# Performance work log

Hardware: AMD Instinct MI355X
Metric: run time of the kernel (lower is better)

Reference implementation:

```python
import jax, jax.numpy as jnp
import numpy as np
from jax import lax

# model dims (must match init_kwargs)
NB, E, G0, G1 = 1, 64, 32, 256          # num_blocks, embed_dim, grid rows, grid cols
DM, DIN, DS, DC, DTR = 2048, 4096, 16, 4, 128  # d_model, d_inner, d_state, d_conv, dt_rank
PS, ST, KD = (2, 16), (2, 16), (31, 31)
B, C, T = 8, 64, 4096


def setup_inputs() -> dict:
    key = jax.random.key(0)
    ks = jax.random.split(key, 4)
    rng = np.random.default_rng(0)

    def w(*s, fan=None):
        fan = fan if fan is not None else s[-1]
        return jnp.asarray((rng.standard_normal(s) / np.sqrt(fan)).astype(np.float32))

    # mamba_ssm-style dt bias init: softplus(bias) ~ Uniform-log in [1e-3, 0.1]
    dt = np.exp(rng.uniform(size=(NB, 2, DIN)) * (np.log(0.1) - np.log(1e-3)) + np.log(1e-3))
    dt = np.clip(dt, 1e-4, None)
    bdt = jnp.asarray((dt + np.log(-np.expm1(-dt))).astype(np.float32))
    A_log = jnp.asarray(np.broadcast_to(np.log(np.arange(1, DS + 1, dtype=np.float32)), (NB, 2, DIN, DS)).copy())

    return {
        'x': jax.random.normal(ks[0], (B, C, T), dtype=jnp.float32),
        'mask': jax.random.uniform(ks[1], (B, C, T)) < 0.5,
        'proj_w': w(E, 1, PS[0], PS[1], fan=PS[0] * PS[1]),
        'proj_b': jnp.zeros((E,), jnp.float32),
        'pos_embed': 0.02 * jax.random.normal(ks[2], (1, G1, DM), dtype=jnp.float32),
        'in_proj_w': w(NB, 2, 2 * DIN, DM, fan=DM),
        'conv_w': w(NB, 2, DIN, DC, fan=DC),
        'conv_b': jnp.zeros((NB, 2, DIN), jnp.float32),
        'x_proj_w': w(NB, 2, DTR + 2 * DS, DIN, fan=DIN),
        'dt_proj_w': w(NB, 2, DIN, DTR, fan=DTR),
        'dt_proj_b': bdt,
        'A_log': A_log,
        'Dp': jnp.ones((NB, 2, DIN), jnp.float32),
        'out_proj_w': w(NB, 2, DM, DIN, fan=DIN),
        'ln_g': jnp.ones((NB, DM), jnp.float32),
        'ln_b': jnp.zeros((NB, DM), jnp.float32),
        'dec_conv_w': w(1, 1, KD[0], KD[1], fan=KD[0] * KD[1]),
        'convT_w': w(E, 1, PS[0], PS[1], fan=E),
        'convT_b': jnp.zeros((1,), jnp.float32),
    }


def _layernorm(x, g, b, eps=1e-5):
    m = jnp.mean(x, -1, keepdims=True)
    v = jnp.var(x, -1, keepdims=True)
    return (x - m) * lax.rsqrt(v + eps) * g + b


def _mamba(h, Win, Wc, bc, Wx, Wdt, bdt, Alog, Dp, Wout):
    # h: [B, L, DM]; faithful port of mamba_ssm Mamba (selective scan reference path)
    xz = jnp.einsum('bld,ed->ble', h, Win)               # [B, L, 2*DIN]
    xc, z = jnp.split(xz, 2, axis=-1)
    xc = xc.swapaxes(1, 2)                               # [B, DIN, L]
    xc = lax.conv_general_dilated(xc, Wc[:, None, :], (1,), ((DC - 1, 0),),
                                  dimension_numbers=('NCH', 'OIH', 'NCH'),
                                  feature_group_count=DIN) + bc[None, :, None]
    u = jax.nn.silu(xc).swapaxes(1, 2)                   # [B, L, DIN]
    x_dbl = jnp.einsum('bld,ed->ble', u, Wx)             # [B, L, DTR+2*DS]
    dt = jax.nn.softplus(jnp.einsum('blr,dr->bld', x_dbl[..., :DTR], Wdt) + bdt)
    Bm = x_dbl[..., DTR:DTR + DS]                        # [B, L, DS]
    Cm = x_dbl[..., DTR + DS:]                           # [B, L, DS]
    A = -jnp.exp(Alog)                                   # [DIN, DS]

    def step(hst, inp):
        dt_t, B_t, C_t, u_t = inp                        # [B,DIN],[B,DS],[B,DS],[B,DIN]
        dA = jnp.exp(dt_t[..., None] * A)                # [B, DIN, DS]
        hst = hst * dA + (dt_t * u_t)[..., None] * B_t[:, None, :]
        return hst, jnp.einsum('bds,bs->bd', hst, C_t)

    h0 = jnp.zeros((h.shape[0], DIN, DS), h.dtype)
    xs = (dt.swapaxes(0, 1), Bm.swapaxes(0, 1), Cm.swapaxes(0, 1), u.swapaxes(0, 1))
    _, ys = lax.scan(step, h0, xs)
    y = ys.swapaxes(0, 1) + u * Dp                       # [B, L, DIN]
    y = y * jax.nn.silu(z)
    return jnp.einsum('bld,ed->ble', y, Wout)            # [B, L, DM]


def _forward(x, mask, proj_w, proj_b, pos_embed, in_proj_w, conv_w, conv_b,
             x_proj_w, dt_proj_w, dt_proj_b, A_log, Dp, out_proj_w,
             ln_g, ln_b, dec_conv_w, convT_w, convT_b):
    xm = jnp.where(mask, 0.0, x)                         # x_masked[mask] = 0
    p = lax.conv_general_dilated(xm[:, None], proj_w, ST, 'VALID',
                                 dimension_numbers=('NCHW', 'OIHW', 'NCHW'))
    p = p + proj_b[None, :, None, None]                  # [B, E, G0, G1]
    h = p.reshape(p.shape[0], E * G0, G1).transpose(0, 2, 1) + pos_embed  # [B, G1, DM]
    for i in range(NB):
        a_f = (in_proj_w[i, 0], conv_w[i, 0], conv_b[i, 0], x_proj_w[i, 0], dt_proj_w[i, 0],
               dt_proj_b[i, 0], A_log[i, 0], Dp[i, 0], out_proj_w[i, 0])
        a_r = (in_proj_w[i, 1], conv_w[i, 1], conv_b[i, 1], x_proj_w[i, 1], dt_proj_w[i, 1],
               dt_proj_b[i, 1], A_log[i, 1], Dp[i, 1], out_proj_w[i, 1])
        o = _mamba(h, *a_f) + jnp.flip(_mamba(jnp.flip(h, 1), *a_r), 1)  # bidirectional add
        h = _layernorm(h + o, ln_g[i], ln_b[i])
    # Decoder
    d = lax.conv_general_dilated(h[:, None], dec_conv_w, (1, 1),
                                 (((KD[0] - 1) // 2,) * 2, ((KD[1] - 1) // 2,) * 2),
                                 dimension_numbers=('NCHW', 'OIHW', 'NCHW'))
    d = d[:, 0].transpose(0, 2, 1).reshape(-1, E, G0, G1)
    # ConvTranspose2d(E->1, k=PS, stride=ST) as lhs-dilated conv with flipped kernel
    wct = jnp.flip(convT_w, (2, 3)).swapaxes(0, 1)       # [1, E, kh, kw]
    rec = lax.conv_general_dilated(d, wct, (1, 1),
                                   ((PS[0] - 1, PS[0] - 1), (PS[1] - 1, PS[1] - 1)),
                                   lhs_dilation=ST,
                                   dimension_numbers=('NCHW', 'OIHW', 'NCHW'))
    rec = rec + convT_b[None, :, None, None]
    return rec[:, 0], x                                  # (x_reconstructed, x_original)


def reference(x, mask, proj_w, proj_b, pos_embed, in_proj_w, conv_w, conv_b,
              x_proj_w, dt_proj_w, dt_proj_b, A_log, Dp, out_proj_w,
              ln_g, ln_b, dec_conv_w, convT_w, convT_b):
    return _forward(x, mask, proj_w, proj_b, pos_embed, in_proj_w, conv_w, conv_b,
                    x_proj_w, dt_proj_w, dt_proj_b, A_log, Dp, out_proj_w,
                    ln_g, ln_b, dec_conv_w, convT_w, convT_b)
```

## Files before the change

### kernel.cpp

```cpp
#include <hip/hip_runtime.h>
#include <hip/hip_bf16.h>
#include <math.h>

typedef unsigned short u16;
typedef __attribute__((ext_vector_type(8))) short bf16x8;
typedef __attribute__((ext_vector_type(4))) float f32x4;

__device__ __forceinline__ float b2f(u16 v) {
  unsigned u = ((unsigned)v) << 16;
  return __builtin_bit_cast(float, u);
}
__device__ __forceinline__ u16 f2b(float f) {
  unsigned u = __builtin_bit_cast(unsigned, f);
  unsigned r = u + 0x7fffu + ((u >> 16) & 1u);
  return (u16)(r >> 16);
}
__device__ __forceinline__ void gload_lds16(const u16* g, u16* l) {
  __builtin_amdgcn_global_load_lds(
      (const __attribute__((address_space(1))) void*)g,
      (__attribute__((address_space(3))) void*)l, 16, 0, 0);
}

__global__ __launch_bounds__(256) void cvt_bf16_k(const float* __restrict__ s,
                                                  u16* __restrict__ d, int n4) {
  int i = blockIdx.x * 256 + threadIdx.x;
  if (i < n4) {
    float4 v = ((const float4*)s)[i];
    ushort4 o;
    o.x = f2b(v.x); o.y = f2b(v.y); o.z = f2b(v.z); o.w = f2b(v.w);
    ((ushort4*)d)[i] = o;
  }
}

__global__ __launch_bounds__(256) void patchify_k(
    const float* __restrict__ x, const int* __restrict__ mask,
    const float* __restrict__ pw, const float* __restrict__ pb,
    const float* __restrict__ pos, float* __restrict__ h, u16* __restrict__ hb)
{
  int g1 = blockIdx.x, b = blockIdx.y, tid = threadIdx.x;
  __shared__ float sX[64 * 17];
  __shared__ float sW[2048];
  for (int i = tid; i < 64 * 16; i += 256) {
    int r = i >> 4, c = i & 15;
    int gi = (b * 64 + r) * 4096 + g1 * 16 + c;
    sX[r * 17 + c] = mask[gi] ? 0.f : x[gi];
  }
  for (int i = tid; i < 2048; i += 256) sW[i] = pw[i];
  __syncthreads();
  for (int m = tid; m < 2048; m += 256) {
    int e = m >> 5, g0 = m & 31;
    float acc = pb[e];
    const float* w = &sW[e * 32];
#pragma unroll
    for (int kh = 0; kh < 2; ++kh)
#pragma unroll
      for (int kw = 0; kw < 16; ++kw)
        acc += sX[(2 * g0 + kh) * 17 + kw] * w[kh * 16 + kw];
    float v = acc + pos[g1 * 2048 + m];
    long o = ((long)b * 256 + g1) * 2048 + m;
    h[o] = v;
    hb[o] = f2b(v);
  }
}

__global__ __launch_bounds__(512, 2) void gemm256_k(
    const u16* __restrict__ A0,
    const u16* __restrict__ B0, long bStride,
    u16* __restrict__ C0, long cStride,
    const float* __restrict__ cw,
    const float* __restrict__ cb,
    u16* __restrict__ ub)
{
  constexpr int K = 2048, N = 8192, LDA = 2048;
  __shared__ __align__(16) u16 lds[67584];
  u16* As = lds;
  u16* Bs = lds + 32768;
  const int dir = blockIdx.z;
  const u16* A = A0;
  const u16* B = B0 + (long)dir * bStride;
  u16* C = C0 + (long)dir * cStride;
  const int flip = dir;

  const int tid = threadIdx.x;
  const int wave = tid >> 6, lane = tid & 63;
  const int wr = wave >> 2, wc = wave & 3;
  const int bm = blockIdx.y * 256, bn = blockIdx.x * 256;
  const int lr = lane & 15, lq = lane >> 4;

  f32x4 acc[8][4];
#pragma unroll
  for (int i = 0; i < 8; ++i)
#pragma unroll
    for (int j = 0; j < 4; ++j) acc[i][j] = (f32x4){0.f, 0.f, 0.f, 0.f};

  auto stage = [&](int buf, int kt) {
    int k0 = kt << 6;
#pragma unroll
    for (int hf = 0; hf < 2; ++hf)
#pragma unroll
      for (int j = 0; j < 2; ++j) {
        int g = j * 512 + tid;
        int rl = hf * 128 + (g >> 3);
        int gr = (g & 7) ^ ((g >> 3) & 7);
        int ar = flip ? (bm + 255 - rl) : (bm + rl);
        gload_lds16(A + (long)ar * LDA + k0 + gr * 8,
                    &As[buf * 16384 + hf * 8192 + g * 8]);
        gload_lds16(B + (long)(bn + rl) * K + k0 + gr * 8,
                    &Bs[buf * 16384 + hf * 8192 + g * 8]);
      }
  };

  const int nk = K >> 6;
  stage(0, 0);
  for (int kt = 0; kt < nk; ++kt) {
    __builtin_amdgcn_s_barrier();
    __builtin_amdgcn_sched_barrier(0);
    if (kt + 1 < nk) {
      stage((kt + 1) & 1, kt + 1);
      asm volatile("s_waitcnt vmcnt(16)" ::: "memory");
    } else {
      asm volatile("s_waitcnt vmcnt(0)" ::: "memory");
    }
    __builtin_amdgcn_sched_barrier(0);
    __builtin_amdgcn_s_barrier();
    __builtin_amdgcn_sched_barrier(0);
    const int buf = kt & 1;
#pragma unroll
    for (int h = 0; h < 2; ++h) {
      bf16x8 av[8], bv[4];
#pragma unroll
      for (int i = 0; i < 8; ++i) {
        int row = wr * 128 + i * 16 + lr;
        av[i] = *(const bf16x8*)
            &As[buf * 16384 + ((row * 64 + h * 32 + lq * 8) ^ ((row & 7) << 3))];
      }
#pragma unroll
      for (int j = 0; j < 4; ++j) {
        int row = wc * 64 + j * 16 + lr;
        bv[j] = *(const bf16x8*)
            &Bs[buf * 16384 + ((row * 64 + h * 32 + lq * 8) ^ ((row & 7) << 3))];
      }
      __builtin_amdgcn_s_setprio(1);
#pragma unroll
      for (int i = 0; i < 8; ++i)
#pragma unroll
        for (int j = 0; j < 4; ++j)
          acc[i][j] = __builtin_amdgcn_mfma_f32_16x16x32_bf16(
              av[i], bv[j], acc[i][j], 0, 0, 0);
      __builtin_amdgcn_s_setprio(0);
    }
  }

  if (bn < 4096) {
    __syncthreads();
    u16* tile = lds;
#pragma unroll
    for (int i = 0; i < 8; ++i) {
      int r0 = wr * 128 + i * 16 + lq * 4;
#pragma unroll
      for (int j = 0; j < 4; ++j) {
        int col = wc * 64 + j * 16 + lr;
        f32x4 v = acc[i][j];
#pragma unroll
        for (int r = 0; r < 4; ++r)
          tile[(r0 + r) * 264 + col] = f2b(v[r]);
      }
    }
    __syncthreads();
    const int rgrp = tid >> 5, c8 = tid & 31;
    const int d0 = bn + c8 * 8;
    float wv0[8], wv1[8], wv2[8], wv3[8], cbv[8];
#pragma unroll
    for (int e = 0; e < 8; ++e) {
      const float4 wq = *(const float4*)(cw + ((long)dir * 4096 + d0 + e) * 4);
      wv0[e] = wq.x; wv1[e] = wq.y; wv2[e] = wq.z; wv3[e] = wq.w;
      cbv[e] = cb[dir * 4096 + d0 + e];
    }
    const int l0 = rgrp * 16;
    float w0[8], w1[8], w2[8];
#pragma unroll
    for (int e = 0; e < 8; ++e) { w0[e] = 0.f; w1[e] = 0.f; w2[e] = 0.f; }
    if (rgrp > 0) {
      bf16x8 t0 = *(const bf16x8*)&tile[(l0 - 3) * 264 + c8 * 8];
      bf16x8 t1 = *(const bf16x8*)&tile[(l0 - 2) * 264 + c8 * 8];
      bf16x8 t2 = *(const bf16x8*)&tile[(l0 - 1) * 264 + c8 * 8];
#pragma unroll
      for (int e = 0; e < 8; ++e) {
        w0[e] = b2f((u16)t0[e]); w1[e] = b2f((u16)t1[e]); w2[e] = b2f((u16)t2[e]);
      }
    }
    long ubase = ((long)(dir * 8 + blockIdx.y) * 256 + l0) * 4096 + d0;
#pragma unroll
    for (int l = 0; l < 16; ++l) {
      bf16x8 t = *(const bf16x8*)&tile[(l0 + l) * 264 + c8 * 8];
      float cur[8];
#pragma unroll
      for (int e = 0; e < 8; ++e) cur[e] = b2f((u16)t[e]);
      bf16x8 ov;
#pragma unroll
      for (int e = 0; e < 8; ++e) {
        float a = cbv[e] + wv0[e] * w0[e] + wv1[e] * w1[e] + wv2[e] * w2[e] +
                  wv3[e] * cur[e];
        ov[e] = (short)f2b(a / (1.f + __expf(-a)));
      }
      *(bf16x8*)(ub + ubase + (long)l * 4096) = ov;
#pragma unroll
      for (int e = 0; e < 8; ++e) { w0[e] = w1[e]; w1[e] = w2[e]; w2[e] = cur[e]; }
    }
  } else {
#pragma unroll
    for (int i = 0; i < 8; ++i) {
      int r0 = bm + wr * 128 + i * 16 + lq * 4;
#pragma unroll
      for (int j = 0; j < 4; ++j) {
        int col = bn + wc * 64 + j * 16 + lr;
        f32x4 v = acc[i][j];
#pragma unroll
        for (int r = 0; r < 4; ++r)
          C[(long)(r0 + r) * N + col] = f2b(v[r]);
      }
    }
  }
}

template <int EPI, int F32OUT, int BFOUT>
__global__ __launch_bounds__(256) void mfma_gemm_k(
    const u16* __restrict__ A0, long aStride,
    const u16* __restrict__ B0, long bStride,
    float* __restrict__ C0, long cStride,
    u16* __restrict__ Cb0, long cbStride,
    const float* __restrict__ bias0, int biasStride,
    int N, int K, int lda, int flipDir1)
{
  __shared__ __align__(16) u16 As[2][4096];
  __shared__ __align__(16) u16 Bs[2][4096];
  const int dir = blockIdx.z;
  const u16* A = A0 + (long)dir * aStride;
  const u16* B = B0 + (long)dir * bStride;
  float* C = F32OUT ? (C0 + (long)dir * cStride) : nullptr;
  u16* Cb = BFOUT ? (Cb0 + (long)dir * cbStride) : nullptr;
  const float* bias = (EPI == 1) ? (bias0 + (long)dir * biasStride) : nullptr;
  const int flip = flipDir1 && (dir == 1);

  const int tid = threadIdx.x;
  const int wave = tid >> 6, lane = tid & 63;
  const int wr = wave >> 1, wc = wave & 1;
  const int bm = blockIdx.y * 128, bn = blockIdx.x * 128;
  const int lr = lane & 15, lq = lane >> 4;

  f32x4 acc[4][4];
#pragma unroll
  for (int i = 0; i < 4; ++i)
#pragma unroll
    for (int j = 0; j < 4; ++j) acc[i][j] = (f32x4){0.f, 0.f, 0.f, 0.f};

  const int nk = K >> 5;

  auto stage = [&](int buf, int k0) {
#pragma unroll
    for (int iss = 0; iss < 2; ++iss) {
      int ob = wave * 2048 + iss * 1024 + lane * 16;
      int row = ob >> 6, kb = (ob >> 4) & 3;
      int rg = bm + row;
      rg = flip ? ((rg & ~255) | (255 - (rg & 255))) : rg;
      gload_lds16(A + (long)rg * lda + k0 + kb * 8,
                  &As[buf][wave * 1024 + iss * 512]);
      int rb = bn + row; rb = (rb < N) ? rb : (N - 1);
      gload_lds16(B + (long)rb * K + k0 + kb * 8,
                  &Bs[buf][wave * 1024 + iss * 512]);
    }
  };

  stage(0, 0);
  for (int kt = 0; kt < nk; ++kt) {
    __syncthreads();
    if (kt + 1 < nk) stage((kt + 1) & 1, (kt + 1) << 5);
    const int buf = kt & 1;
    bf16x8 av[4], bv[4];
#pragma unroll
    for (int i = 0; i < 4; ++i)
      av[i] = *(const bf16x8*)&As[buf][(wr * 64 + i * 16 + lr) * 32 + lq * 8];
#pragma unroll
    for (int j = 0; j < 4; ++j)
      bv[j] = *(const bf16x8*)&Bs[buf][(wc * 64 + j * 16 + lr) * 32 + lq * 8];
#pragma unroll
    for (int i = 0; i < 4; ++i)
#pragma unroll
      for (int j = 0; j < 4; ++j)
        acc[i][j] = __builtin_amdgcn_mfma_f32_16x16x32_bf16(av[i], bv[j],
                                                            acc[i][j], 0, 0, 0);
  }

#pragma unroll
  for (int i = 0; i < 4; ++i) {
    int r0 = bm + wr * 64 + i * 16 + lq * 4;
#pragma unroll
    for (int j = 0; j < 4; ++j) {
      int col = bn + wc * 64 + j * 16 + lr;
      if (col < N) {
        f32x4 v = acc[i][j];
#pragma unroll
        for (int r = 0; r < 4; ++r) {
          float xv = v[r];
          if (EPI == 1) {
            xv += bias[col];
            xv = (xv > 20.f) ? xv : log1pf(expf(xv));
          }
          if (F32OUT) C[(long)(r0 + r) * N + col] = xv;
          if (BFOUT) Cb[(long)(r0 + r) * N + col] = f2b(xv);
        }
      }
    }
  }
}

__global__ __launch_bounds__(256) void xdbl_part_k(
    const u16* __restrict__ ubf, const u16* __restrict__ Wxbf,
    float* __restrict__ part)
{
  __shared__ __align__(16) u16 As[2][4096];
  __shared__ __align__(16) u16 Bs[2][4096];
  const int dir = blockIdx.z >> 2, split = blockIdx.z & 3;
  const u16* A = ubf + (long)dir * 2048 * 4096;
  const u16* B = Wxbf + (long)dir * 160 * 4096;
  float* C = part + (long)blockIdx.z * 327680;
  const int tid = threadIdx.x;
  const int wave = tid >> 6, lane = tid & 63;
  const int wr = wave >> 1, wc = wave & 1;
  const int bm = blockIdx.y * 128, bn = blockIdx.x * 128;
  const int lr = lane & 15, lq = lane >> 4;

  f32x4 acc[4][4];
#pragma unroll
  for (int i = 0; i < 4; ++i)
#pragma unroll
    for (int j = 0; j < 4; ++j) acc[i][j] = (f32x4){0.f, 0.f, 0.f, 0.f};

  auto stage = [&](int buf, int k0) {
#pragma unroll
    for (int iss = 0; iss < 2; ++iss) {
      int ob = wave * 2048 + iss * 1024 + lane * 16;
      int row = ob >> 6, kb = (ob >> 4) & 3;
      gload_lds16(A + (long)(bm + row) * 4096 + k0 + kb * 8,
                  &As[buf][wave * 1024 + iss * 512]);
      int rb = bn + row; rb = (rb < 160) ? rb : 159;
      gload_lds16(B + (long)rb * 4096 + k0 + kb * 8,
                  &Bs[buf][wave * 1024 + iss * 512]);
    }
  };

  const int kbase = split << 10;
  stage(0, kbase);
  for (int kt = 0; kt < 32; ++kt) {
    __syncthreads();
    if (kt + 1 < 32) stage((kt + 1) & 1, kbase + ((kt + 1) << 5));
    const int buf = kt & 1;
    bf16x8 av[4], bv[4];
#pragma unroll
    for (int i = 0; i < 4; ++i)
      av[i] = *(const bf16x8*)&As[buf][(wr * 64 + i * 16 + lr) * 32 + lq * 8];
#pragma unroll
    for (int j = 0; j < 4; ++j)
      bv[j] = *(const bf16x8*)&Bs[buf][(wc * 64 + j * 16 + lr) * 32 + lq * 8];
#pragma unroll
    for (int i = 0; i < 4; ++i)
#pragma unroll
      for (int j = 0; j < 4; ++j)
        acc[i][j] = __builtin_amdgcn_mfma_f32_16x16x32_bf16(av[i], bv[j],
                                                            acc[i][j], 0, 0, 0);
  }

#pragma unroll
  for (int i = 0; i < 4; ++i) {
    int r0 = bm + wr * 64 + i * 16 + lq * 4;
#pragma unroll
    for (int j = 0; j < 4; ++j) {
      int col = bn + wc * 64 + j * 16 + lr;
      if (col < 160) {
        f32x4 v = acc[i][j];
#pragma unroll
        for (int r = 0; r < 4; ++r)
          C[(long)(r0 + r) * 160 + col] = v[r];
      }
    }
  }
}

__global__ __launch_bounds__(256) void xdbl_reduce_k(
    const float* __restrict__ part, float* __restrict__ xdbl,
    u16* __restrict__ xdbl_bf)
{
  int i = blockIdx.x * 256 + threadIdx.x;
  if (i >= 655360) return;
  int dir = i / 327680, rem = i - dir * 327680;
  long pb = (long)dir * 4 * 327680 + rem;
  float s = part[pb] + part[pb + 327680] + part[pb + 2 * 327680] +
            part[pb + 3 * 327680];
  xdbl[i] = s;
  xdbl_bf[i] = f2b(s);
}

__global__ __launch_bounds__(256) void scan_a_k(
    const u16* __restrict__ dtbuf, const u16* __restrict__ ubuf,
    const float* __restrict__ xdbl, const float* __restrict__ A_log,
    const float* __restrict__ Dpv, u16* __restrict__ ypre,
    float* __restrict__ stend, float* __restrict__ dtsum)
{
  int blk = blockIdx.x;
  int dtile = blk & 15, c = (blk >> 4) & 7, b = (blk >> 7) & 7, dir = blk >> 10;
  int tid = threadIdx.x;
  int d = dtile * 256 + tid;
  int db = dir * 8 + b;

  __shared__ float sB[32][16], sC[32][16];
  long r160 = (long)db * 256 * 160;
  for (int i = tid; i < 1024; i += 256) {
    int l = i >> 5, s = i & 31;
    float v = xdbl[r160 + (long)(c * 32 + l) * 160 + 128 + s];
    if (s < 16) sB[l][s] = v; else sC[l][s - 16] = v;
  }
  __syncthreads();

  float A[16], st[16];
  const float4* ap = (const float4*)(A_log + ((long)dir * 4096 + d) * 16);
#pragma unroll
  for (int q = 0; q < 4; ++q) {
    float4 t = ap[q];
    A[q * 4 + 0] = -__expf(t.x); A[q * 4 + 1] = -__expf(t.y);
    A[q * 4 + 2] = -__expf(t.z); A[q * 4 + 3] = -__expf(t.w);
  }
#pragma unroll
  for (int s = 0; s < 16; ++s) st[s] = 0.f;
  float Dpd = Dpv[dir * 4096 + d];

  long base = (long)db * 256 * 4096 + (long)c * 32 * 4096 + d;
  float dts = 0.f;
  for (int i = 0; i < 32; ++i) {
    float dtv = b2f(dtbuf[base + (long)i * 4096]);
    float uv  = b2f(ubuf[base + (long)i * 4096]);
    dts += dtv;
    float du = dtv * uv;
    float y = 0.f;
#pragma unroll
    for (int s = 0; s < 16; ++s) {
      st[s] = st[s] * __expf(dtv * A[s]) + du * sB[i][s];
      y += st[s] * sC[i][s];
    }
    ypre[base + (long)i * 4096] = f2b(y + uv * Dpd);
  }
  long eb = ((long)(db * 8 + c) * 4096 + d) * 16;
  float4* ep = (float4*)(stend + eb);
#pragma unroll
  for (int q = 0; q < 4; ++q)
    ep[q] = make_float4(st[q * 4], st[q * 4 + 1], st[q * 4 + 2], st[q * 4 + 3]);
  dtsum[(long)(db * 8 + c) * 4096 + d] = dts;
}

__global__ __launch_bounds__(512) void scan_b_k(
    const u16* __restrict__ dtbuf, const u16* __restrict__ xzbf,
    const float* __restrict__ xdbl, const float* __restrict__ A_log,
    const float* __restrict__ stend, const float* __restrict__ dtsum,
    u16* __restrict__ ybuf)
{
  int blk = blockIdx.x;
  int dtile = blk & 63, b = (blk >> 6) & 7, dir = blk >> 9;
  int tid = threadIdx.x;
  int c = tid >> 6, dd = tid & 63;
  int d0 = dtile * 64, d = d0 + dd;
  int db = dir * 8 + b;

  __shared__ float sEnd[8][64][17];
  __shared__ float sT[8][64];
  __shared__ float sC[256][16];

  long eBase = (long)db * 8 * 65536;
  for (int i = tid; i < 8192; i += 512) {
    int cc = i >> 10, rem = i & 1023, dd2 = rem >> 4, s = rem & 15;
    sEnd[cc][dd2][s] = stend[eBase + (long)cc * 65536 + (long)(d0 + dd2) * 16 + s];
  }
  {
    int cc = tid >> 6, dd2 = tid & 63;
    sT[cc][dd2] = dtsum[(long)(db * 8 + cc) * 4096 + d0 + dd2];
  }
  long r160 = (long)db * 256 * 160;
  for (int i = tid; i < 4096; i += 512) {
    int l = i >> 4, s = i & 15;
    sC[l][s] = xdbl[r160 + (long)l * 160 + 144 + s];
  }
  __syncthreads();

  float A[16];
  const float4* ap = (const float4*)(A_log + ((long)dir * 4096 + d) * 16);
#pragma unroll
  for (int q = 0; q < 4; ++q) {
    float4 t = ap[q];
    A[q * 4 + 0] = -__expf(t.x); A[q * 4 + 1] = -__expf(t.y);
    A[q * 4 + 2] = -__expf(t.z); A[q * 4 + 3] = -__expf(t.w);
  }
  float g[16];
#pragma unroll
  for (int s = 0; s < 16; ++s) g[s] = 0.f;
  for (int j = 0; j < c; ++j) {
    float Tj = sT[j][dd];
#pragma unroll
    for (int s = 0; s < 16; ++s)
      g[s] = g[s] * __expf(A[s] * Tj) + sEnd[j][dd][s];
  }

  long base  = (long)db * 256 * 4096 + (long)c * 32 * 4096 + d;
  long zbase = (long)db * 256 * 8192 + (long)c * 32 * 8192 + 4096 + d;
  float cum = 0.f;
  if (c == 0) {
    for (int i = 0; i < 32; ++i) {
      float yp = b2f(ybuf[base + (long)i * 4096]);
      float zv = b2f(xzbf[zbase + (long)i * 8192]);
      float y = yp * (zv / (1.f + __expf(-zv)));
      ybuf[base + (long)i * 4096] = f2b(y);
    }
  } else {
    for (int i = 0; i < 32; ++i) {
      float dtv = b2f(dtbuf[base + (long)i * 4096]);
      cum += dtv;
      float yp = b2f(ybuf[base + (long)i * 4096]);
      float corr = 0.f;
      const int l = c * 32 + i;
#pragma unroll
      for (int s = 0; s < 16; ++s)
        corr += sC[l][s] * __expf(A[s] * cum) * g[s];
      float zv = b2f(xzbf[zbase + (long)i * 8192]);
      float y = (yp + corr) * (zv / (1.f + __expf(-zv)));
      ybuf[base + (long)i * 4096] = f2b(y);
    }
  }
}

__global__ __launch_bounds__(256) void add_ln_k(
    const float* __restrict__ h, const float* __restrict__ o0,
    const float* __restrict__ o1, const float* __restrict__ g,
    const float* __restrict__ bta, float* __restrict__ h2)
{
  int row = blockIdx.x;
  int b = row >> 8, l = row & 255;
  long base = (long)row * 2048;
  long base1 = ((long)b * 256 + (255 - l)) * 2048;
  int t8 = threadIdx.x * 8;
  float v[8];
  float4 x0 = *(const float4*)(h + base + t8);
  float4 x1 = *(const float4*)(h + base + t8 + 4);
  float4 a0 = *(const float4*)(o0 + base + t8);
  float4 a1 = *(const float4*)(o0 + base + t8 + 4);
  float4 c0 = *(const float4*)(o1 + base1 + t8);
  float4 c1 = *(const float4*)(o1 + base1 + t8 + 4);
  v[0] = x0.x + a0.x + c0.x; v[1] = x0.y + a0.y + c0.y;
  v[2] = x0.z + a0.z + c0.z; v[3] = x0.w + a0.w + c0.w;
  v[4] = x1.x + a1.x + c1.x; v[5] = x1.y + a1.y + c1.y;
  v[6] = x1.z + a1.z + c1.z; v[7] = x1.w + a1.w + c1.w;
  float s = 0.f, ss = 0.f;
#pragma unroll
  for (int j = 0; j < 8; ++j) { s += v[j]; ss += v[j] * v[j]; }
#pragma unroll
  for (int off = 32; off >= 1; off >>= 1) {
    s += __shfl_xor(s, off, 64);
    ss += __shfl_xor(ss, off, 64);
  }
  __shared__ float red[8];
  int wid = threadIdx.x >> 6, lane = threadIdx.x & 63;
  if (lane == 0) { red[wid] = s; red[wid + 4] = ss; }
  __syncthreads();
  if (threadIdx.x == 0) {
    red[0] = red[0] + red[1] + red[2] + red[3];
    red[4] = red[4] + red[5] + red[6] + red[7];
  }
  __syncthreads();
  float mean = red[0] * (1.f / 2048.f);
  float var = red[4] * (1.f / 2048.f) - mean * mean;
  float inv = rsqrtf(var + 1e-5f);
  float o[8];
#pragma unroll
  for (int j = 0; j < 8; ++j)
    o[j] = (v[j] - mean) * inv * g[t8 + j] + bta[t8 + j];
  *(float4*)(h2 + base + t8) = make_float4(o[0], o[1], o[2], o[3]);
  *(float4*)(h2 + base + t8 + 4) = make_float4(o[4], o[5], o[6], o[7]);
}

__global__ __launch_bounds__(256) void dec_conv31_k(
    const float* __restrict__ h2, const float* __restrict__ kw,
    float* __restrict__ dc)
{
  __shared__ u16 sIn[62 * 168];
  __shared__ float sKw[961];
  int b = blockIdx.z;
  int l0 = blockIdx.y * 32;
  int m0 = blockIdx.x * 128;
  int tid = threadIdx.x;
  const float* src = h2 + (long)b * 256 * 2048;
  for (int i = tid; i < 961; i += 256) sKw[i] = kw[i];
  for (int i = tid; i < 62 * 168; i += 256) {
    int r = i / 168, c = i - r * 168;
    int gl = l0 + r - 15, gm = m0 + c - 15;
    float v = 0.f;
    if (c < 158 && gl >= 0 && gl < 256 && gm >= 0 && gm < 2048)
      v = src[(long)gl * 2048 + gm];
    sIn[i] = f2b(v);
  }
  __syncthreads();
  int tx = tid & 15, ty = tid >> 4;
  float acc[2][8];
#pragma unroll
  for (int r = 0; r < 2; ++r)
#pragma unroll
    for (int c = 0; c < 8; ++c) acc[r][c] = 0.f;

#pragma unroll 1
  for (int k = 0; k < 32; ++k) {
    const u16* rowp = &sIn[(ty * 2 + k) * 168 + tx * 8];
    float w[40];
#pragma unroll
    for (int q = 0; q < 5; ++q) {
      bf16x8 t = *(const bf16x8*)(rowp + q * 8);
#pragma unroll
      for (int e = 0; e < 8; ++e) w[q * 8 + e] = b2f((u16)t[e]);
    }
#pragma unroll
    for (int r = 0; r < 2; ++r) {
      unsigned ki = (unsigned)(k - r);
      if (ki > 30u) continue;
      const float* kwr = &sKw[ki * 31];
#pragma unroll
      for (int kj = 0; kj < 31; ++kj) {
        float kv = kwr[kj];
#pragma unroll
        for (int c = 0; c < 8; ++c) acc[r][c] += w[kj + c] * kv;
      }
    }
  }
#pragma unroll
  for (int r = 0; r < 2; ++r) {
    long obase = ((long)b * 256 + l0 + ty * 2 + r) * 2048 + m0 + tx * 8;
    *(float4*)(dc + obase) = make_float4(acc[r][0], acc[r][1], acc[r][2], acc[r][3]);
    *(float4*)(dc + obase + 4) = make_float4(acc[r][4], acc[r][5], acc[r][6], acc[r][7]);
  }
}

__global__ __launch_bounds__(256) void convT_k(
    const float* __restrict__ dc, const float* __restrict__ w,
    const float* __restrict__ wb, float* __restrict__ out)
{
  int j = blockIdx.x, b = blockIdx.y;
  __shared__ float sD[2048];
  __shared__ float sW[2048];
  int tid = threadIdx.x;
  const float* drow = dc + ((long)b * 256 + j) * 2048;
  for (int i = tid; i < 2048; i += 256) { sD[i] = drow[i]; sW[i] = w[i]; }
  __syncthreads();
  float cb = wb[0];
  int owlo = tid & 15, ohbase = tid >> 4;
#pragma unroll
  for (int q = 0; q < 4; ++q) {
    int oh = ohbase + q * 16;
    int i = oh >> 1, a = oh & 1;
    float acc = cb;
#pragma unroll 8
    for (int e = 0; e < 64; ++e)
      acc += sD[e * 32 + i] * sW[e * 32 + a * 16 + owlo];
    out[((long)b * 64 + oh) * 4096 + j * 16 + owlo] = acc;
  }
}

extern "C" void kernel_launch(void* const* d_in, const int* in_sizes, int n_in,
                              void* d_out, int out_size, void* d_ws, size_t ws_size,
                              hipStream_t stream)
{
  const float* x      = (const float*)d_in[0];
  const int*   mask   = (const int*)d_in[1];
  const float* proj_w = (const float*)d_in[2];
  const float* proj_b = (const float*)d_in[3];
  const float* pos    = (const float*)d_in[4];
  const float* Wip    = (const float*)d_in[5];
  const float* convw  = (const float*)d_in[6];
  const float* convb  = (const float*)d_in[7];
  const float* Wx     = (const float*)d_in[8];
  const float* Wdt    = (const float*)d_in[9];
  const float* bdt    = (const float*)d_in[10];
  const float* Alog   = (const float*)d_in[11];
  const float* Dpv    = (const float*)d_in[12];
  const float* Wout   = (const float*)d_in[13];
  const float* lng    = (const float*)d_in[14];
  const float* lnb    = (const float*)d_in[15];
  const float* dkw    = (const float*)d_in[16];
  const float* ctw    = (const float*)d_in[17];
  const float* ctb    = (const float*)d_in[18];
  float* out = (float*)d_out;

  char* p = (char*)d_ws;
  u16*   xz_bf   = (u16*)p;
  float* ob      = (float*)p;
  p += 67108864;
  u16*   u_bf    = (u16*)p;
  float* dc      = (float*)p;
  p += 33554432;
  u16*   dt_bf   = (u16*)p; p += 67108864;
  float* xdbl    = (float*)p; p += 2621440;
  u16*   xdbl_bf = (u16*)p;  p += 1310720;
  float* h       = (float*)p; p += 16777216;
  u16*   h_bf    = (u16*)p;  p += 8388608;
  float* h2      = (float*)p; p += 16777216;
  u16*   y_bf    = (u16*)p;  p += 33554432;
  u16*   Wpool   = (u16*)p;  p += 67108864;
  u16*   Wx_bf   = (u16*)p;  p += 2621440;
  u16*   Wdt_bf  = (u16*)p;  p += 2097152;

  float* part   = (float*)(Wpool + 16777216);
  float* st_end = (float*)(Wpool + 16777216);
  float* dtsum  = h2;

  cvt_bf16_k<<<32768, 256, 0, stream>>>(Wip, Wpool, 8388608);
  cvt_bf16_k<<<1280, 256, 0, stream>>>(Wx, Wx_bf, 327680);
  cvt_bf16_k<<<1024, 256, 0, stream>>>(Wdt, Wdt_bf, 262144);

  patchify_k<<<dim3(256, 8), 256, 0, stream>>>(x, mask, proj_w, proj_b, pos, h, h_bf);

  gemm256_k<<<dim3(32, 8, 2), 512, 0, stream>>>(
      h_bf, Wpool, (long)8192 * 2048, xz_bf, (long)2048 * 8192,
      convw, convb, u_bf);

  xdbl_part_k<<<dim3(2, 16, 8), 256, 0, stream>>>(u_bf, Wx_bf, part);
  xdbl_reduce_k<<<2560, 256, 0, stream>>>(part, xdbl, xdbl_bf);

  mfma_gemm_k<1, 0, 1><<<dim3(32, 16, 2), 256, 0, stream>>>(
      xdbl_bf, (long)2048 * 160, Wdt_bf, (long)4096 * 128, nullptr, 0L,
      dt_bf, (long)2048 * 4096, bdt, 4096, 4096, 128, 160, 0);

  scan_a_k<<<2048, 256, 0, stream>>>(dt_bf, u_bf, xdbl, Alog, Dpv, y_bf, st_end, dtsum);
  scan_b_k<<<1024, 512, 0, stream>>>(dt_bf, xz_bf, xdbl, Alog, st_end, dtsum, y_bf);

  cvt_bf16_k<<<16384, 256, 0, stream>>>(Wout, Wpool, 4194304);

  mfma_gemm_k<0, 1, 0><<<dim3(16, 16, 2), 256, 0, stream>>>(
      y_bf, (long)2048 * 4096, Wpool, (long)2048 * 4096, ob, (long)2048 * 2048,
      nullptr, 0L, nullptr, 0, 2048, 4096, 4096, 0);

  add_ln_k<<<2048, 256, 0, stream>>>(h, ob, ob + (long)2048 * 2048, lng, lnb, h2);

  dec_conv31_k<<<dim3(16, 8, 8), 256, 0, stream>>>(h2, dkw, dc);

  convT_k<<<dim3(256, 8), 256, 0, stream>>>(dc, ctw, ctb, out);

  hipMemcpyAsync(out + 2097152, x, (size_t)2097152 * 4,
                 hipMemcpyDeviceToDevice, stream);
}
```

Before: 690.4 us.

## Fuse dt projection GEMM with chunked scan pass and store cumulative dt

The dt_proj GEMM (with bias and softplus) is merged into the first scan kernel. Each 128x128 MFMA tile's softplus output stays in LDS and feeds the per-chunk selective scan directly, so the full bf16 dt tensor is never written and read back. The kernel instead writes a bf16 cumulative-dt array that the second scan pass reads in place of recomputing running sums, which also removes the separate dtsum buffer. Costs: each thread now scans two chunks in sequence with fewer blocks in flight, and the cumulative sums are rounded to bf16, which may lose precision in the correction exponent.

```diff
diff --git a/kernel.cpp b/kernel.cpp
--- a/kernel.cpp
+++ b/kernel.cpp
@@ -400,67 +400,144 @@
   xdbl_bf[i] = f2b(s);
 }
 
-__global__ __launch_bounds__(256) void scan_a_k(
-    const u16* __restrict__ dtbuf, const u16* __restrict__ ubuf,
+__global__ __launch_bounds__(256) void dtscan_k(
+    const u16* __restrict__ xdblbf, const u16* __restrict__ Wdtbf,
+    const float* __restrict__ bdt, const u16* __restrict__ ubuf,
     const float* __restrict__ xdbl, const float* __restrict__ A_log,
     const float* __restrict__ Dpv, u16* __restrict__ ypre,
-    float* __restrict__ stend, float* __restrict__ dtsum)
-{
-  int blk = blockIdx.x;
-  int dtile = blk & 15, c = (blk >> 4) & 7, b = (blk >> 7) & 7, dir = blk >> 10;
-  int tid = threadIdx.x;
-  int d = dtile * 256 + tid;
-  int db = dir * 8 + b;
-
-  __shared__ float sB[32][16], sC[32][16];
+    u16* __restrict__ cumdt, float* __restrict__ stend)
+{
+  __shared__ __align__(16) u16 lds[25088];
+  u16* As = lds;
+  u16* Bs = lds + 8192;
+  const int dir = blockIdx.z;
+  const u16* A = xdblbf + (long)dir * 2048 * 160;
+  const u16* B = Wdtbf + (long)dir * 4096 * 128;
+  const float* bias = bdt + dir * 4096;
+  const int tid = threadIdx.x;
+  const int wave = tid >> 6, lane = tid & 63;
+  const int wr = wave >> 1, wc = wave & 1;
+  const int bm = blockIdx.y * 128, bn = blockIdx.x * 128;
+  const int lr = lane & 15, lq = lane >> 4;
+
+  f32x4 acc[4][4];
+#pragma unroll
+  for (int i = 0; i < 4; ++i)
+#pragma unroll
+    for (int j = 0; j < 4; ++j) acc[i][j] = (f32x4){0.f, 0.f, 0.f, 0.f};
+
+  auto stage = [&](int buf, int k0) {
+#pragma unroll
+    for (int iss = 0; iss < 2; ++iss) {
+      int ob = wave * 2048 + iss * 1024 + lane * 16;
+      int row = ob >> 6, kb = (ob >> 4) & 3;
+      gload_lds16(A + (long)(bm + row) * 160 + k0 + kb * 8,
+                  &As[buf * 4096 + wave * 1024 + iss * 512]);
+      gload_lds16(B + (long)(bn + row) * 128 + k0 + kb * 8,
+                  &Bs[buf * 4096 + wave * 1024 + iss * 512]);
+    }
+  };
+
+  stage(0, 0);
+  for (int kt = 0; kt < 4; ++kt) {
+    __syncthreads();
+    if (kt + 1 < 4) stage((kt + 1) & 1, (kt + 1) << 5);
+    const int buf = kt & 1;
+    bf16x8 av[4], bv[4];
+#pragma unroll
+    for (int i = 0; i < 4; ++i)
+      av[i] = *(const bf16x8*)&As[buf * 4096 + (wr * 64 + i * 16 + lr) * 32 + lq * 8];
+#pragma unroll
+    for (int j = 0; j < 4; ++j)
+      bv[j] = *(const bf16x8*)&Bs[buf * 4096 + (wc * 64 + j * 16 + lr) * 32 + lq * 8];
+#pragma unroll
+    for (int i = 0; i < 4; ++i)
+#pragma unroll
+      for (int j = 0; j < 4; ++j)
+        acc[i][j] = __builtin_amdgcn_mfma_f32_16x16x32_bf16(av[i], bv[j],
+                                                            acc[i][j], 0, 0, 0);
+  }
+
+  __syncthreads();
+  u16* tile = lds;
+  float* sB = (float*)(lds + 16896);
+  float* sC = sB + 2048;
+#pragma unroll
+  for (int i = 0; i < 4; ++i) {
+    int r0 = wr * 64 + i * 16 + lq * 4;
+#pragma unroll
+    for (int j = 0; j < 4; ++j) {
+      int col = wc * 64 + j * 16 + lr;
+      f32x4 v = acc[i][j];
+#pragma unroll
+      for (int r = 0; r < 4; ++r) {
+        float xv = v[r] + bias[bn + col];
+        xv = (xv > 20.f) ? xv : log1pf(expf(xv));
+        tile[(r0 + r) * 132 + col] = f2b(xv);
+      }
+    }
+  }
+
+  const int db = dir * 8 + (bm >> 8);
+  const int l0 = bm & 255;
+  const int c0 = l0 >> 5;
   long r160 = (long)db * 256 * 160;
-  for (int i = tid; i < 1024; i += 256) {
-    int l = i >> 5, s = i & 31;
-    float v = xdbl[r160 + (long)(c * 32 + l) * 160 + 128 + s];
-    if (s < 16) sB[l][s] = v; else sC[l][s - 16] = v;
+  for (int i2 = tid; i2 < 2048; i2 += 256) {
+    int row = i2 >> 4, s = i2 & 15;
+    float2 bc = *(const float2*)&xdbl[r160 + (long)(l0 + row) * 160 + 128 + s * 2];
+    (void)bc;
+    sB[row * 16 + s] = xdbl[r160 + (long)(l0 + row) * 160 + 128 + s];
+    sC[row * 16 + s] = xdbl[r160 + (long)(l0 + row) * 160 + 144 + s];
   }
   __syncthreads();
 
-  float A[16], st[16];
-  const float4* ap = (const float4*)(A_log + ((long)dir * 4096 + d) * 16);
+  const int d_loc = tid & 127, half = tid >> 7;
+  const int d_glob = bn + d_loc;
+  float Aa[16];
+  const float4* ap = (const float4*)(A_log + ((long)dir * 4096 + d_glob) * 16);
 #pragma unroll
   for (int q = 0; q < 4; ++q) {
     float4 t = ap[q];
-    A[q * 4 + 0] = -__expf(t.x); A[q * 4 + 1] = -__expf(t.y);
-    A[q * 4 + 2] = -__expf(t.z); A[q * 4 + 3] = -__expf(t.w);
-  }
-#pragma unroll
-  for (int s = 0; s < 16; ++s) st[s] = 0.f;
-  float Dpd = Dpv[dir * 4096 + d];
-
-  long base = (long)db * 256 * 4096 + (long)c * 32 * 4096 + d;
-  float dts = 0.f;
-  for (int i = 0; i < 32; ++i) {
-    float dtv = b2f(dtbuf[base + (long)i * 4096]);
-    float uv  = b2f(ubuf[base + (long)i * 4096]);
-    dts += dtv;
-    float du = dtv * uv;
-    float y = 0.f;
-#pragma unroll
-    for (int s = 0; s < 16; ++s) {
-      st[s] = st[s] * __expf(dtv * A[s]) + du * sB[i][s];
-      y += st[s] * sC[i][s];
-    }
-    ypre[base + (long)i * 4096] = f2b(y + uv * Dpd);
-  }
-  long eb = ((long)(db * 8 + c) * 4096 + d) * 16;
-  float4* ep = (float4*)(stend + eb);
-#pragma unroll
-  for (int q = 0; q < 4; ++q)
-    ep[q] = make_float4(st[q * 4], st[q * 4 + 1], st[q * 4 + 2], st[q * 4 + 3]);
-  dtsum[(long)(db * 8 + c) * 4096 + d] = dts;
+    Aa[q * 4 + 0] = -__expf(t.x); Aa[q * 4 + 1] = -__expf(t.y);
+    Aa[q * 4 + 2] = -__expf(t.z); Aa[q * 4 + 3] = -__expf(t.w);
+  }
+  float Dpd = Dpv[dir * 4096 + d_glob];
+
+#pragma unroll
+  for (int pass = 0; pass < 2; ++pass) {
+    const int c = c0 + half + pass * 2;
+    const int lrow0 = (half + pass * 2) * 32;
+    long base = (long)db * 256 * 4096 + (long)c * 32 * 4096 + d_glob;
+    float st[16];
+#pragma unroll
+    for (int s = 0; s < 16; ++s) st[s] = 0.f;
+    float cum = 0.f;
+    for (int i = 0; i < 32; ++i) {
+      float dtv = b2f(tile[(lrow0 + i) * 132 + d_loc]);
+      float uv = b2f(ubuf[base + (long)i * 4096]);
+      cum += dtv;
+      cumdt[base + (long)i * 4096] = f2b(cum);
+      float du = dtv * uv;
+      float y = 0.f;
+#pragma unroll
+      for (int s = 0; s < 16; ++s) {
+        st[s] = st[s] * __expf(dtv * Aa[s]) + du * sB[(lrow0 + i) * 16 + s];
+        y += st[s] * sC[(lrow0 + i) * 16 + s];
+      }
+      ypre[base + (long)i * 4096] = f2b(y + uv * Dpd);
+    }
+    long eb = ((long)(db * 8 + c) * 4096 + d_glob) * 16;
+    float4* ep = (float4*)(stend + eb);
+#pragma unroll
+    for (int q = 0; q < 4; ++q)
+      ep[q] = make_float4(st[q * 4], st[q * 4 + 1], st[q * 4 + 2], st[q * 4 + 3]);
+  }
 }
 
 __global__ __launch_bounds__(512) void scan_b_k(
-    const u16* __restrict__ dtbuf, const u16* __restrict__ xzbf,
+    const u16* __restrict__ cumdt, const u16* __restrict__ xzbf,
     const float* __restrict__ xdbl, const float* __restrict__ A_log,
-    const float* __restrict__ stend, const float* __restrict__ dtsum,
-    u16* __restrict__ ybuf)
+    const float* __restrict__ stend, u16* __restrict__ ybuf)
 {
   int blk = blockIdx.x;
   int dtile = blk & 63, b = (blk >> 6) & 7, dir = blk >> 9;
@@ -480,7 +557,7 @@
   }
   {
     int cc = tid >> 6, dd2 = tid & 63;
-    sT[cc][dd2] = dtsum[(long)(db * 8 + cc) * 4096 + d0 + dd2];
+    sT[cc][dd2] = b2f(cumdt[((long)db * 256 + cc * 32 + 31) * 4096 + d0 + dd2]);
   }
   long r160 = (long)db * 256 * 160;
   for (int i = tid; i < 4096; i += 512) {
@@ -509,7 +586,6 @@
 
   long base  = (long)db * 256 * 4096 + (long)c * 32 * 4096 + d;
   long zbase = (long)db * 256 * 8192 + (long)c * 32 * 8192 + 4096 + d;
-  float cum = 0.f;
   if (c == 0) {
     for (int i = 0; i < 32; ++i) {
       float yp = b2f(ybuf[base + (long)i * 4096]);
@@ -519,8 +595,7 @@
     }
   } else {
     for (int i = 0; i < 32; ++i) {
-      float dtv = b2f(dtbuf[base + (long)i * 4096]);
-      cum += dtv;
+      float cum = b2f(cumdt[base + (long)i * 4096]);
       float yp = b2f(ybuf[base + (long)i * 4096]);
       float corr = 0.f;
       const int l = c * 32 + i;
@@ -699,7 +774,7 @@
   u16*   u_bf    = (u16*)p;
   float* dc      = (float*)p;
   p += 33554432;
-  u16*   dt_bf   = (u16*)p; p += 67108864;
+  u16*   cumdt_bf= (u16*)p; p += 67108864;
   float* xdbl    = (float*)p; p += 2621440;
   u16*   xdbl_bf = (u16*)p;  p += 1310720;
   float* h       = (float*)p; p += 16777216;
@@ -712,7 +787,6 @@
 
   float* part   = (float*)(Wpool + 16777216);
   float* st_end = (float*)(Wpool + 16777216);
-  float* dtsum  = h2;
 
   cvt_bf16_k<<<32768, 256, 0, stream>>>(Wip, Wpool, 8388608);
   cvt_bf16_k<<<1280, 256, 0, stream>>>(Wx, Wx_bf, 327680);
@@ -727,12 +801,10 @@
   xdbl_part_k<<<dim3(2, 16, 8), 256, 0, stream>>>(u_bf, Wx_bf, part);
   xdbl_reduce_k<<<2560, 256, 0, stream>>>(part, xdbl, xdbl_bf);
 
-  mfma_gemm_k<1, 0, 1><<<dim3(32, 16, 2), 256, 0, stream>>>(
-      xdbl_bf, (long)2048 * 160, Wdt_bf, (long)4096 * 128, nullptr, 0L,
-      dt_bf, (long)2048 * 4096, bdt, 4096, 4096, 128, 160, 0);
-
-  scan_a_k<<<2048, 256, 0, stream>>>(dt_bf, u_bf, xdbl, Alog, Dpv, y_bf, st_end, dtsum);
-  scan_b_k<<<1024, 512, 0, stream>>>(dt_bf, xz_bf, xdbl, Alog, st_end, dtsum, y_bf);
+  dtscan_k<<<dim3(32, 16, 2), 256, 0, stream>>>(
+      xdbl_bf, Wdt_bf, bdt, u_bf, xdbl, Alog, Dpv, y_bf, cumdt_bf, st_end);
+
+  scan_b_k<<<1024, 512, 0, stream>>>(cumdt_bf, xz_bf, xdbl, Alog, st_end, y_bf);
 
   cvt_bf16_k<<<16384, 256, 0, stream>>>(Wout, Wpool, 4194304);
 
```

Result: no change. 698.6 us (+1.2%).

## Compute decoder 31x31 conv with MFMA via Toeplitz-expanded kernel matrix

Applied to the files above, without the earlier changes.

Rewrites the 31x31 decoder convolution as a sequence of bf16 MFMA matrix products. Each kernel row is expanded into a banded Toeplitz matrix by a new small prep kernel, and input tiles are staged in LDS as bf16. This replaces the scalar FMA loop with matrix-core instructions and changes the tile to 64x64. The cost is redundant multiplies by the zero bands of the Toeplitz matrix, plus one extra tiny kernel launch.

```diff
diff --git a/kernel.cpp b/kernel.cpp
--- a/kernel.cpp
+++ b/kernel.cpp
@@ -30,6 +30,17 @@
     o.x = f2b(v.x); o.y = f2b(v.y); o.z = f2b(v.z); o.w = f2b(v.w);
     ((ushort4*)d)[i] = o;
   }
+}
+
+__global__ __launch_bounds__(256) void toeplitz_k(
+    const float* __restrict__ kw, u16* __restrict__ tb)
+{
+  int i = blockIdx.x * 256 + threadIdx.x;
+  if (i >= 31744) return;
+  int k = i & 31, n = (i >> 5) & 15, h = (i >> 9) & 1, ki = i >> 10;
+  int t = h * 32 + k - n;
+  float v = (t >= 0 && t <= 30) ? kw[ki * 31 + t] : 0.f;
+  tb[i] = f2b(v);
 }
 
 __global__ __launch_bounds__(256) void patchify_k(
@@ -584,61 +595,51 @@
 }
 
 __global__ __launch_bounds__(256) void dec_conv31_k(
-    const float* __restrict__ h2, const float* __restrict__ kw,
+    const float* __restrict__ h2, const u16* __restrict__ tb,
     float* __restrict__ dc)
 {
-  __shared__ u16 sIn[62 * 168];
-  __shared__ float sKw[961];
-  int b = blockIdx.z;
-  int l0 = blockIdx.y * 32;
-  int m0 = blockIdx.x * 128;
-  int tid = threadIdx.x;
+  __shared__ __align__(16) u16 sIn[94 * 120];
+  const int b = blockIdx.z;
+  const int l0 = blockIdx.y * 64;
+  const int m0 = blockIdx.x * 64;
+  const int tid = threadIdx.x;
   const float* src = h2 + (long)b * 256 * 2048;
-  for (int i = tid; i < 961; i += 256) sKw[i] = kw[i];
-  for (int i = tid; i < 62 * 168; i += 256) {
-    int r = i / 168, c = i - r * 168;
+  for (int i = tid; i < 94 * 112; i += 256) {
+    int r = i / 112, c = i - r * 112;
     int gl = l0 + r - 15, gm = m0 + c - 15;
     float v = 0.f;
-    if (c < 158 && gl >= 0 && gl < 256 && gm >= 0 && gm < 2048)
+    if (gl >= 0 && gl < 256 && gm >= 0 && gm < 2048)
       v = src[(long)gl * 2048 + gm];
-    sIn[i] = f2b(v);
+    sIn[r * 120 + c] = f2b(v);
   }
   __syncthreads();
-  int tx = tid & 15, ty = tid >> 4;
-  float acc[2][8];
-#pragma unroll
-  for (int r = 0; r < 2; ++r)
-#pragma unroll
-    for (int c = 0; c < 8; ++c) acc[r][c] = 0.f;
+  const int wave = tid >> 6, lane = tid & 63;
+  const int lr = lane & 15, lq = lane >> 4;
+
+  f32x4 acc[4];
+#pragma unroll
+  for (int s = 0; s < 4; ++s) acc[s] = (f32x4){0.f, 0.f, 0.f, 0.f};
 
 #pragma unroll 1
-  for (int k = 0; k < 32; ++k) {
-    const u16* rowp = &sIn[(ty * 2 + k) * 168 + tx * 8];
-    float w[40];
-#pragma unroll
-    for (int q = 0; q < 5; ++q) {
-      bf16x8 t = *(const bf16x8*)(rowp + q * 8);
-#pragma unroll
-      for (int e = 0; e < 8; ++e) w[q * 8 + e] = b2f((u16)t[e]);
-    }
-#pragma unroll
-    for (int r = 0; r < 2; ++r) {
-      unsigned ki = (unsigned)(k - r);
-      if (ki > 30u) continue;
-      const float* kwr = &sKw[ki * 31];
-#pragma unroll
-      for (int kj = 0; kj < 31; ++kj) {
-        float kv = kwr[kj];
-#pragma unroll
-        for (int c = 0; c < 8; ++c) acc[r][c] += w[kj + c] * kv;
-      }
-    }
-  }
-#pragma unroll
-  for (int r = 0; r < 2; ++r) {
-    long obase = ((long)b * 256 + l0 + ty * 2 + r) * 2048 + m0 + tx * 8;
-    *(float4*)(dc + obase) = make_float4(acc[r][0], acc[r][1], acc[r][2], acc[r][3]);
-    *(float4*)(dc + obase + 4) = make_float4(acc[r][4], acc[r][5], acc[r][6], acc[r][7]);
+  for (int ki = 0; ki < 31; ++ki) {
+    const u16* arow = &sIn[(wave * 16 + lr + ki) * 120];
+#pragma unroll
+    for (int h = 0; h < 2; ++h) {
+      bf16x8 bv = *(const bf16x8*)&tb[((ki * 2 + h) * 16 + lr) * 32 + lq * 8];
+#pragma unroll
+      for (int ms = 0; ms < 4; ++ms) {
+        bf16x8 av = *(const bf16x8*)&arow[ms * 16 + h * 32 + lq * 8];
+        acc[ms] = __builtin_amdgcn_mfma_f32_16x16x32_bf16(av, bv, acc[ms], 0, 0, 0);
+      }
+    }
+  }
+#pragma unroll
+  for (int ms = 0; ms < 4; ++ms) {
+    f32x4 v = acc[ms];
+#pragma unroll
+    for (int r = 0; r < 4; ++r)
+      dc[((long)b * 256 + l0 + wave * 16 + lq * 4 + r) * 2048 + m0 + ms * 16 + lr]
+          = v[r];
   }
 }
 
@@ -709,6 +710,7 @@
   u16*   Wpool   = (u16*)p;  p += 67108864;
   u16*   Wx_bf   = (u16*)p;  p += 2621440;
   u16*   Wdt_bf  = (u16*)p;  p += 2097152;
+  u16*   tb      = (u16*)p;  p += 65536;
 
   float* part   = (float*)(Wpool + 16777216);
   float* st_end = (float*)(Wpool + 16777216);
@@ -717,6 +719,7 @@
   cvt_bf16_k<<<32768, 256, 0, stream>>>(Wip, Wpool, 8388608);
   cvt_bf16_k<<<1280, 256, 0, stream>>>(Wx, Wx_bf, 327680);
   cvt_bf16_k<<<1024, 256, 0, stream>>>(Wdt, Wdt_bf, 262144);
+  toeplitz_k<<<124, 256, 0, stream>>>(dkw, tb);
 
   patchify_k<<<dim3(256, 8), 256, 0, stream>>>(x, mask, proj_w, proj_b, pos, h, h_bf);
 
@@ -742,7 +745,7 @@
 
   add_ln_k<<<2048, 256, 0, stream>>>(h, ob, ob + (long)2048 * 2048, lng, lnb, h2);
 
-  dec_conv31_k<<<dim3(16, 8, 8), 256, 0, stream>>>(h2, dkw, dc);
+  dec_conv31_k<<<dim3(32, 4, 8), 256, 0, stream>>>(h2, tb, dc);
 
   convT_k<<<dim3(256, 8), 256, 0, stream>>>(dc, ctw, ctb, out);
 
```

Measured after the change: 636.6 us. 1.08x faster.
